# Performance work log

Measured on AMD Instinct MI355X. Metric: run time of the kernel, lower is better.

Reference implementation:

```python
import jax, jax.numpy as jnp
import numpy as np
from jax import lax

B, H, W = 8, 2048, 2048

def _conv3x3(x, w):
    # x: [B,H,W,1], w: [3,3,1,1] (HWIO), SAME padding, stride 1
    return lax.conv_general_dilated(
        x, w, window_strides=(1, 1), padding='SAME',
        dimension_numbers=('NHWC', 'HWIO', 'NHWC'))

def setup_inputs() -> dict:
    key = jax.random.key(0)
    k1, k2, k3, k4, k5, k6 = jax.random.split(key, 6)
    x = jax.random.normal(k1, (B, H, W, 1), dtype=jnp.float32)
    mask = jax.random.randint(k2, (B, H, W, 1), 0, 2, dtype=jnp.int32)
    w1 = jax.random.normal(k3, (3, 3, 1, 1), dtype=jnp.float32)
    b1 = jax.random.normal(k4, (1,), dtype=jnp.float32)
    w2 = jax.random.normal(k5, (3, 3, 1, 1), dtype=jnp.float32)
    b2 = jax.random.normal(k6, (1,), dtype=jnp.float32)
    return {"x": x, "mask": mask, "w1": w1, "b1": b1, "w2": w2, "b2": b2}

def reference(x, mask, w1, b1, w2, b2):
    # Stride-1 MinkowskiConvolution on a sparse 2D tensor == dense 3x3 conv over
    # features zeroed at unoccupied coords, with bias + output restricted to the
    # occupied coordinate set (out_coords == in_coords for stride 1).
    m = mask.astype(x.dtype)                       # occupancy [B,H,W,1]
    h = (_conv3x3(x * m, w1) + b1) * m             # conv1 + bias on active coords
    h = jax.nn.relu(h)                             # MinkowskiReLU (per active coord)
    out = (_conv3x3(h, w2) + b2) * m               # conv2 + bias on active coords
    return out
```

## Files before the change

### kernel.cpp

```cpp
#include <hip/hip_runtime.h>


#define TB_W 128
#define TB_H 16
#define SX   136
#define SY   20
#define NV4  (SX / 4)
#define NSTG (SY * NV4)
#define HX   130
#define HY   18
#define NH   (HX * HY)

__global__ __launch_bounds__(256) void fused_mconv2(
    const float* __restrict__ x, const int* __restrict__ mask,
    const float* __restrict__ w1p, const float* __restrict__ b1p,
    const float* __restrict__ w2p, const float* __restrict__ b2p,
    float* __restrict__ out, int H, int W)
{
    __shared__ float s_xm[SY][SX];
    __shared__ float s_hm[SY][SX];

    const int tid  = threadIdx.y * 64 + threadIdx.x;
    const int c0   = blockIdx.x * TB_W;
    const int row0 = blockIdx.y * TB_H;
    const size_t plane = (size_t)H * W;
    const float* xb = x    + (size_t)blockIdx.z * plane;
    const int*   mb = mask + (size_t)blockIdx.z * plane;
    float*       ob = out  + (size_t)blockIdx.z * plane;

    float W1[9], W2[9];
    #pragma unroll
    for (int i = 0; i < 9; ++i) { W1[i] = w1p[i]; W2[i] = w2p[i]; }
    const float B1 = b1p[0], B2 = b2p[0];

    for (int idx = tid; idx < NSTG; idx += 256) {
        const int row  = idx / NV4;
        const int col4 = idx - row * NV4;
        const int r = row0 - 2 + row;
        const int c = c0 - 4 + (col4 << 2);
        float4 xm = make_float4(0.f, 0.f, 0.f, 0.f);
        float4 mm = make_float4(0.f, 0.f, 0.f, 0.f);
        if (r >= 0 && r < H && c >= 0 && c < W) {
            const size_t g = (size_t)r * W + c;
            const float4 xv = *reinterpret_cast<const float4*>(xb + g);
            const int4   mi = *reinterpret_cast<const int4*>(mb + g);
            mm = make_float4((float)mi.x, (float)mi.y, (float)mi.z, (float)mi.w);
            xm = make_float4(xv.x * mm.x, xv.y * mm.y, xv.z * mm.z, xv.w * mm.w);
        }
        *reinterpret_cast<float4*>(&s_xm[row][col4 << 2]) = xm;
        *reinterpret_cast<float4*>(&s_hm[row][col4 << 2]) = mm;
    }
    __syncthreads();

    for (int idx = tid; idx < NH; idx += 256) {
        const int hrow = idx / HX;
        const int hcol = idx - hrow * HX;
        const float m = s_hm[hrow + 1][hcol + 3];
        float acc = B1;
        #pragma unroll
        for (int di = 0; di < 3; ++di)
            #pragma unroll
            for (int dj = 0; dj < 3; ++dj)
                acc += W1[di * 3 + dj] * s_xm[hrow + di][hcol + 2 + dj];
        const float h = acc > 0.f ? acc : 0.f;
        s_hm[hrow + 1][hcol + 3] = (m > 0.5f) ? h : -1.0f;
    }
    __syncthreads();

    {
        const int j     = tid & 127;
        const int strip = tid >> 7;
        const int i0    = strip * (TB_H / 2);
        float P = 0.f, Q = 0.f, cm = 0.f;
        #pragma unroll
        for (int t = 1; t <= TB_H / 2 + 2; ++t) {
            const int s = i0 + t;
            const float* rowp = &s_hm[s][0];
            const float t0 = rowp[j + 3];
            const float t1 = rowp[j + 4];
            const float t2 = rowp[j + 5];
            const float r0 = t0 > 0.f ? t0 : 0.f;
            const float r1 = t1 > 0.f ? t1 : 0.f;
            const float r2 = t2 > 0.f ? t2 : 0.f;
            const float d0 = W2[0] * r0 + W2[1] * r1 + W2[2] * r2;
            const float d1 = W2[3] * r0 + W2[4] * r1 + W2[5] * r2;
            const float d2 = W2[6] * r0 + W2[7] * r1 + W2[8] * r2;
            if (t >= 3) {
                const int i = s - 3;
                const float v = (cm >= 0.f) ? (Q + d2 + B2) : 0.f;
                ob[(size_t)(row0 + i) * W + (c0 + j)] = v;
            }
            Q  = P + d1;
            P  = d0;
            cm = t1;
        }
    }
}

extern "C" void kernel_launch(void* const* d_in, const int* in_sizes, int n_in,
                              void* d_out, int out_size, void* d_ws, size_t ws_size,
                              hipStream_t stream) {
    const float* x    = (const float*)d_in[0];
    const int*   mask = (const int*)  d_in[1];
    const float* w1   = (const float*)d_in[2];
    const float* b1   = (const float*)d_in[3];
    const float* w2   = (const float*)d_in[4];
    const float* b2   = (const float*)d_in[5];
    float*       out  = (float*)d_out;

    const int H = 2048, W = 2048;
    const int B = in_sizes[0] / (H * W);

    dim3 block(64, 4, 1);
    dim3 grid(W / TB_W, H / TB_H, B);
    hipLaunchKernelGGL(fused_mconv2, grid, block, 0, stream,
                       x, mask, w1, b1, w2, b2, out, H, W);
}
```

Baseline: 86.24 us.

## Vectorize conv stages to two outputs per thread and re-read mask from global

Each thread in the first conv stage now computes two adjacent hidden values from float2 shared loads, and each thread in the second stage emits two adjacent outputs with a float2 global store. The staged mask array is removed: masking in staging becomes a select, and the hidden-stage mask is re-read from global (cache-resident) memory. This cuts shared-memory traffic, LDS footprint and per-element instruction count. In exchange it adds scalar global mask loads in the middle stage and uses 6-row strips per thread, so the 2-row halo is recomputed per strip.

```diff
diff --git a/kernel.cpp b/kernel.cpp
--- a/kernel.cpp
+++ b/kernel.cpp
@@ -9,7 +9,9 @@
 #define NSTG (SY * NV4)
 #define HX   130
 #define HY   18
-#define NH   (HX * HY)
+#define HP   (HX / 2)
+#define NH2  (HY * HP)
+#define SHX  132
 
 __global__ __launch_bounds__(256) void fused_mconv2(
     const float* __restrict__ x, const int* __restrict__ mask,
@@ -17,8 +19,8 @@
     const float* __restrict__ w2p, const float* __restrict__ b2p,
     float* __restrict__ out, int H, int W)
 {
-    __shared__ float s_xm[SY][SX];
-    __shared__ float s_hm[SY][SX];
+    __shared__ __align__(16) float s_xm[SY][SX];
+    __shared__ __align__(16) float s_h [HY][SHX];
 
     const int tid  = threadIdx.y * 64 + threadIdx.x;
     const int c0   = blockIdx.x * TB_W;
@@ -39,60 +41,79 @@
         const int r = row0 - 2 + row;
         const int c = c0 - 4 + (col4 << 2);
         float4 xm = make_float4(0.f, 0.f, 0.f, 0.f);
-        float4 mm = make_float4(0.f, 0.f, 0.f, 0.f);
         if (r >= 0 && r < H && c >= 0 && c < W) {
             const size_t g = (size_t)r * W + c;
             const float4 xv = *reinterpret_cast<const float4*>(xb + g);
             const int4   mi = *reinterpret_cast<const int4*>(mb + g);
-            mm = make_float4((float)mi.x, (float)mi.y, (float)mi.z, (float)mi.w);
-            xm = make_float4(xv.x * mm.x, xv.y * mm.y, xv.z * mm.z, xv.w * mm.w);
+            xm.x = mi.x ? xv.x : 0.f;
+            xm.y = mi.y ? xv.y : 0.f;
+            xm.z = mi.z ? xv.z : 0.f;
+            xm.w = mi.w ? xv.w : 0.f;
         }
         *reinterpret_cast<float4*>(&s_xm[row][col4 << 2]) = xm;
-        *reinterpret_cast<float4*>(&s_hm[row][col4 << 2]) = mm;
     }
     __syncthreads();
 
-    for (int idx = tid; idx < NH; idx += 256) {
-        const int hrow = idx / HX;
-        const int hcol = idx - hrow * HX;
-        const float m = s_hm[hrow + 1][hcol + 3];
-        float acc = B1;
+    for (int idx = tid; idx < NH2; idx += 256) {
+        const int hrow = idx / HP;
+        const int hp   = idx - hrow * HP;
+        const int hc   = hp << 1;
+        float acc0 = B1, acc1 = B1;
         #pragma unroll
-        for (int di = 0; di < 3; ++di)
-            #pragma unroll
-            for (int dj = 0; dj < 3; ++dj)
-                acc += W1[di * 3 + dj] * s_xm[hrow + di][hcol + 2 + dj];
-        const float h = acc > 0.f ? acc : 0.f;
-        s_hm[hrow + 1][hcol + 3] = (m > 0.5f) ? h : -1.0f;
+        for (int di = 0; di < 3; ++di) {
+            const float2 a = *reinterpret_cast<const float2*>(&s_xm[hrow + di][hc + 2]);
+            const float2 b = *reinterpret_cast<const float2*>(&s_xm[hrow + di][hc + 4]);
+            acc0 += W1[di * 3] * a.x + W1[di * 3 + 1] * a.y + W1[di * 3 + 2] * b.x;
+            acc1 += W1[di * 3] * a.y + W1[di * 3 + 1] * b.x + W1[di * 3 + 2] * b.y;
+        }
+        const int r = row0 - 1 + hrow;
+        int m0 = 0, m1 = 0;
+        if (r >= 0 && r < H) {
+            const int* rowm = mb + (size_t)r * W;
+            const int ca = c0 - 1 + hc;
+            if (ca >= 0)    m0 = rowm[ca];
+            if (ca + 1 < W) m1 = rowm[ca + 1];
+        }
+        float2 enc;
+        const float h0 = acc0 > 0.f ? acc0 : 0.f;
+        const float h1 = acc1 > 0.f ? acc1 : 0.f;
+        enc.x = m0 ? h0 : -1.0f;
+        enc.y = m1 ? h1 : -1.0f;
+        *reinterpret_cast<float2*>(&s_h[hrow][hc]) = enc;
     }
     __syncthreads();
 
     {
-        const int j     = tid & 127;
-        const int strip = tid >> 7;
-        const int i0    = strip * (TB_H / 2);
-        float P = 0.f, Q = 0.f, cm = 0.f;
+        const int p     = tid & 63;
+        const int strip = tid >> 6;
+        const int j     = p << 1;
+        const int hr0   = strip << 2;
+        float P0 = 0.f, Q0 = 0.f, cm0 = 0.f;
+        float P1 = 0.f, Q1 = 0.f, cm1 = 0.f;
         #pragma unroll
-        for (int t = 1; t <= TB_H / 2 + 2; ++t) {
-            const int s = i0 + t;
-            const float* rowp = &s_hm[s][0];
-            const float t0 = rowp[j + 3];
-            const float t1 = rowp[j + 4];
-            const float t2 = rowp[j + 5];
-            const float r0 = t0 > 0.f ? t0 : 0.f;
-            const float r1 = t1 > 0.f ? t1 : 0.f;
-            const float r2 = t2 > 0.f ? t2 : 0.f;
-            const float d0 = W2[0] * r0 + W2[1] * r1 + W2[2] * r2;
-            const float d1 = W2[3] * r0 + W2[4] * r1 + W2[5] * r2;
-            const float d2 = W2[6] * r0 + W2[7] * r1 + W2[8] * r2;
-            if (t >= 3) {
-                const int i = s - 3;
-                const float v = (cm >= 0.f) ? (Q + d2 + B2) : 0.f;
-                ob[(size_t)(row0 + i) * W + (c0 + j)] = v;
+        for (int t = 0; t < 6; ++t) {
+            const int hr = hr0 + t;
+            const float2 a = *reinterpret_cast<const float2*>(&s_h[hr][j]);
+            const float2 b = *reinterpret_cast<const float2*>(&s_h[hr][j + 2]);
+            const float r0 = a.x > 0.f ? a.x : 0.f;
+            const float r1 = a.y > 0.f ? a.y : 0.f;
+            const float r2 = b.x > 0.f ? b.x : 0.f;
+            const float r3 = b.y > 0.f ? b.y : 0.f;
+            const float d00 = W2[0] * r0 + W2[1] * r1 + W2[2] * r2;
+            const float d10 = W2[3] * r0 + W2[4] * r1 + W2[5] * r2;
+            const float d20 = W2[6] * r0 + W2[7] * r1 + W2[8] * r2;
+            const float d01 = W2[0] * r1 + W2[1] * r2 + W2[2] * r3;
+            const float d11 = W2[3] * r1 + W2[4] * r2 + W2[5] * r3;
+            const float d21 = W2[6] * r1 + W2[7] * r2 + W2[8] * r3;
+            if (t >= 2) {
+                const int i = hr - 2;
+                float2 o;
+                o.x = (cm0 >= 0.f) ? (Q0 + d20 + B2) : 0.f;
+                o.y = (cm1 >= 0.f) ? (Q1 + d21 + B2) : 0.f;
+                *reinterpret_cast<float2*>(ob + (size_t)(row0 + i) * W + (c0 + j)) = o;
             }
-            Q  = P + d1;
-            P  = d0;
-            cm = t1;
+            Q0 = P0 + d10; P0 = d00; cm0 = a.y;
+            Q1 = P1 + d11; P1 = d01; cm1 = b.x;
         }
     }
 }
```

New measurement: 115.1 us. 33.4% more time.
